# Optimization experiments

Measured on AMD Instinct MI355X. Metric: run time of the kernel, lower is better.

Reference implementation:

```python
import jax, jax.numpy as jnp
from jax import lax
import numpy as np

D_MODEL = 1024
D_STATE = 16
D_CONV = 4
EXPAND = 2
D_INNER = EXPAND * D_MODEL          # 2048
DT_RANK = D_MODEL // 16             # 64 (mamba 'auto' dt_rank)
B, L = 1, 1024


def setup_inputs() -> dict:
    key = jax.random.key(0)
    ks = jax.random.split(key, 8)

    def nrm(k, shape, s=0.02):
        return jax.random.normal(k, shape, jnp.float32) * s

    def mamba_params(kbase):
        k = jax.random.split(kbase, 7)
        return {
            'in_w': nrm(k[0], (2 * D_INNER, D_MODEL)),            # in_proj (no bias)
            'conv_w': nrm(k[1], (D_INNER, 1, D_CONV), 0.1),       # depthwise causal conv
            'conv_b': nrm(k[2], (D_INNER,), 0.1),
            'xproj_w': nrm(k[3], (DT_RANK + 2 * D_STATE, D_INNER)),
            'dt_w': nrm(k[4], (D_INNER, DT_RANK), 0.1),
            'dt_b': nrm(k[5], (D_INNER,), 0.1),
            'Alog': jnp.log(jnp.broadcast_to(jnp.arange(1., D_STATE + 1, dtype=jnp.float32), (D_INNER, D_STATE))),
            'Dp': jnp.ones((D_INNER,), jnp.float32),
            'out_w': nrm(k[6], (D_MODEL, D_INNER)),
        }

    fw = mamba_params(ks[0])
    bw = mamba_params(ks[1])
    inp = {'x': jax.random.normal(ks[2], (B, L, D_MODEL), jnp.float32)}
    for n, p in fw.items():
        inp['fw_' + n] = p
    for n, p in bw.items():
        inp['bw_' + n] = p
    inp['proj_w'] = nrm(ks[3], (D_MODEL, 2 * D_MODEL))
    inp['proj_b'] = jnp.zeros((D_MODEL,), jnp.float32)
    inp['ln_w'] = jnp.ones((D_MODEL,), jnp.float32)
    inp['ln_b'] = jnp.zeros((D_MODEL,), jnp.float32)
    return inp


def _mamba(x, in_w, conv_w, conv_b, xproj_w, dt_w, dt_b, Alog, Dp, out_w):
    # x: [B, L, d_model]
    xz = x @ in_w.T                                    # [B, L, 2*d_inner]
    xi, z = jnp.split(xz, 2, axis=-1)
    # causal depthwise conv over time
    xc = lax.conv_general_dilated(jnp.swapaxes(xi, 1, 2), conv_w, (1,),
                                  [(D_CONV - 1, 0)], feature_group_count=D_INNER)
    u = jnp.swapaxes(jax.nn.silu(xc + conv_b[None, :, None]), 1, 2)   # [B, L, d_inner]
    x_dbl = u @ xproj_w.T                              # [B, L, dt_rank + 2*d_state]
    dt = x_dbl[..., :DT_RANK]
    Bm = x_dbl[..., DT_RANK:DT_RANK + D_STATE]
    Cm = x_dbl[..., DT_RANK + D_STATE:]
    delta = jax.nn.softplus(dt @ dt_w.T + dt_b)        # [B, L, d_inner]
    A = -jnp.exp(Alog)                                 # [d_inner, d_state]
    dA = jnp.exp(jnp.einsum('bld,dn->bldn', delta, A))
    dBu = jnp.einsum('bld,bln,bld->bldn', delta, Bm, u)

    def step(h, inputs):
        a, b, c = inputs                               # a,b: [B,D,N]; c: [B,N]
        h = a * h + b
        return h, jnp.einsum('bdn,bn->bd', h, c)

    h0 = jnp.zeros((x.shape[0], D_INNER, D_STATE), x.dtype)
    _, ys = lax.scan(step, h0, (jnp.moveaxis(dA, 1, 0), jnp.moveaxis(dBu, 1, 0), jnp.moveaxis(Cm, 1, 0)))
    y = jnp.moveaxis(ys, 0, 1) + u * Dp                # [B, L, d_inner]
    return (y * jax.nn.silu(z)) @ out_w.T              # [B, L, d_model]


def _block(x,
           fw_in_w, fw_conv_w, fw_conv_b, fw_xproj_w, fw_dt_w, fw_dt_b, fw_Alog, fw_Dp, fw_out_w,
           bw_in_w, bw_conv_w, bw_conv_b, bw_xproj_w, bw_dt_w, bw_dt_b, bw_Alog, bw_Dp, bw_out_w,
           proj_w, proj_b, ln_w, ln_b):
    out_fw = _mamba(x, fw_in_w, fw_conv_w, fw_conv_b, fw_xproj_w, fw_dt_w, fw_dt_b, fw_Alog, fw_Dp, fw_out_w) + x
    xb = jnp.flip(x, axis=1)
    out_bw = jnp.flip(_mamba(xb, bw_in_w, bw_conv_w, bw_conv_b, bw_xproj_w, bw_dt_w, bw_dt_b, bw_Alog, bw_Dp, bw_out_w) + xb, axis=1)
    out = jnp.concatenate([out_fw, out_bw], axis=-1) @ proj_w.T + proj_b
    mu = out.mean(-1, keepdims=True)
    var = out.var(-1, keepdims=True)
    return (out - mu) / jnp.sqrt(var + 1e-5) * ln_w + ln_b


def reference(x,
              fw_in_w, fw_conv_w, fw_conv_b, fw_xproj_w, fw_dt_w, fw_dt_b, fw_Alog, fw_Dp, fw_out_w,
              bw_in_w, bw_conv_w, bw_conv_b, bw_xproj_w, bw_dt_w, bw_dt_b, bw_Alog, bw_Dp, bw_out_w,
              proj_w, proj_b, ln_w, ln_b):
    return _block(x,
                  fw_in_w, fw_conv_w, fw_conv_b, fw_xproj_w, fw_dt_w, fw_dt_b, fw_Alog, fw_Dp, fw_out_w,
                  bw_in_w, bw_conv_w, bw_conv_b, bw_xproj_w, bw_dt_w, bw_dt_b, bw_Alog, bw_Dp, bw_out_w,
                  proj_w, proj_b, ln_w, ln_b)
```

## Files before the change

### kernel.cpp

```cpp
#include <hip/hip_runtime.h>

typedef __bf16 bf16;
typedef __bf16 bf16x8 __attribute__((ext_vector_type(8)));
typedef float  f32x4  __attribute__((ext_vector_type(4)));

#define L_SEQ 1024
#define DM    1024
#define DI    2048
#define DTR   64
#define DSTATE 16
#define XD    96
#define NC    64
#define CS    16

__device__ __forceinline__ float bf2f(bf16 v){ return (float)v; }
__device__ __forceinline__ bf16  f2bf(float v){ return (bf16)v; }

__device__ __forceinline__ void gl_lds16(const bf16* g, bf16* l) {
  __builtin_amdgcn_global_load_lds(
      (const __attribute__((address_space(1))) unsigned int*)g,
      (__attribute__((address_space(3))) unsigned int*)l, 16, 0, 0);
}

#define OFF_X      0L
#define OFF_INW    1048576L
#define OFF_XPROJ  9437184L
#define OFF_DTW    9830400L
#define OFF_OUTW   10092544L
#define OFF_PROJW  14286848L
#define CVT_TOTAL  16384000L

__global__ __launch_bounds__(256) void cvt_k(
    const float* __restrict__ x,
    const float* __restrict__ inw0, const float* __restrict__ inw1,
    const float* __restrict__ xp0,  const float* __restrict__ xp1,
    const float* __restrict__ dt0,  const float* __restrict__ dt1,
    const float* __restrict__ ow0,  const float* __restrict__ ow1,
    const float* __restrict__ pw,   bf16* __restrict__ wb)
{
  long i = ((long)blockIdx.x * 256 + threadIdx.x) * 8;
  if (i >= CVT_TOTAL) return;
  const float* src; long off;
  if      (i < OFF_INW)                 { src = x;    off = i - OFF_X; }
  else if (i < OFF_INW + 4194304L)      { src = inw0; off = i - OFF_INW; }
  else if (i < OFF_XPROJ)               { src = inw1; off = i - (OFF_INW + 4194304L); }
  else if (i < OFF_XPROJ + 196608L)     { src = xp0;  off = i - OFF_XPROJ; }
  else if (i < OFF_DTW)                 { src = xp1;  off = i - (OFF_XPROJ + 196608L); }
  else if (i < OFF_DTW + 131072L)       { src = dt0;  off = i - OFF_DTW; }
  else if (i < OFF_OUTW)                { src = dt1;  off = i - (OFF_DTW + 131072L); }
  else if (i < OFF_OUTW + 2097152L)     { src = ow0;  off = i - OFF_OUTW; }
  else if (i < OFF_PROJW)               { src = ow1;  off = i - (OFF_OUTW + 2097152L); }
  else                                  { src = pw;   off = i - OFF_PROJW; }
  f32x4 v0 = *(const f32x4*)(src + off);
  f32x4 v1 = *(const f32x4*)(src + off + 4);
  bf16x8 t;
  #pragma unroll
  for (int q = 0; q < 4; q++) { t[q] = (bf16)v0[q]; t[4+q] = (bf16)v1[q]; }
  *(bf16x8*)(wb + i) = t;
}

template<int BM, int BN>
__global__ __launch_bounds__(256) void gemm_bt(
    const bf16* __restrict__ A, const bf16* __restrict__ B0, const bf16* __restrict__ B1,
    void* __restrict__ Cv, void* __restrict__ Cv2, int splitN,
    int M, int N, int K, int lda, int ldb, int ldc,
    long aOffZ, long cOffZ,
    const float* __restrict__ bias0, const float* __restrict__ bias1,
    int flipA1, int writeBf16, int act,
    const float* __restrict__ xF, int fuseRes)
{
  constexpr int WM = BM / 2, WN = BN / 2;
  constexpr int MI = WM / 16, NJ = WN / 16;
  constexpr int ACALLS = BM / 32;
  constexpr int BCALLS = BN / 32;

  const int tid  = threadIdx.x;
  const int z    = blockIdx.z;
  const bf16*  Bp   = z ? B1 : B0;
  const float* bias = z ? bias1 : bias0;
  const int flip = z ? flipA1 : 0;
  const int bm = blockIdx.x * BM;
  const int bn = blockIdx.y * BN;

  __shared__ bf16 As[BM * 64];
  __shared__ bf16 Bs[BN * 64];

  f32x4 acc[MI][NJ];
  #pragma unroll
  for (int i=0;i<MI;i++)
    #pragma unroll
    for (int j=0;j<NJ;j++) { acc[i][j][0]=0.f; acc[i][j][1]=0.f; acc[i][j][2]=0.f; acc[i][j][3]=0.f; }

  const int wave = tid >> 6;
  const int lane = tid & 63;
  const int wm = (wave >> 1) * WM;
  const int wn = (wave & 1) * WN;
  const int fr  = lane & 15;
  const int frx = fr & 7;
  const int kqc = lane >> 4;

  const bf16* aSrc[ACALLS];
  int aOff[ACALLS];
  #pragma unroll
  for (int t = 0; t < ACALLS; t++) {
    int s = (wave * ACALLS + t) * 64 + lane;
    int r = s >> 3;
    int j = (s & 7) ^ (r & 7);
    int ar = bm + r;
    int agr = flip ? (M - 1 - ar) : ar;
    aSrc[t] = A + (long)z * aOffZ + (long)agr * lda + j * 8;
    aOff[t] = (wave * ACALLS + t) * 512;
  }
  const bf16* bSrc[BCALLS];
  int bOff[BCALLS];
  #pragma unroll
  for (int t = 0; t < BCALLS; t++) {
    int s = (wave * BCALLS + t) * 64 + lane;
    int r = s >> 3;
    int j = (s & 7) ^ (r & 7);
    int br = bn + r; if (br > N - 1) br = N - 1;
    bSrc[t] = Bp + (long)br * ldb + j * 8;
    bOff[t] = (wave * BCALLS + t) * 512;
  }

  for (int k0 = 0; k0 < K; k0 += 64) {
    #pragma unroll
    for (int t = 0; t < ACALLS; t++) gl_lds16(aSrc[t] + k0, &As[aOff[t]]);
    #pragma unroll
    for (int t = 0; t < BCALLS; t++) gl_lds16(bSrc[t] + k0, &Bs[bOff[t]]);
    __syncthreads();

    #pragma unroll
    for (int ks8 = 0; ks8 < 8; ks8 += 4) {
      bf16x8 af[MI], bfr[NJ];
      #pragma unroll
      for (int i=0;i<MI;i++) {
        int row = wm + i*16 + fr;
        af[i]  = *(const bf16x8*)&As[(row * 8 + ((ks8 + kqc) ^ frx)) * 8];
      }
      #pragma unroll
      for (int j=0;j<NJ;j++) {
        int row = wn + j*16 + fr;
        bfr[j] = *(const bf16x8*)&Bs[(row * 8 + ((ks8 + kqc) ^ frx)) * 8];
      }
      #pragma unroll
      for (int i=0;i<MI;i++)
        #pragma unroll
        for (int j=0;j<NJ;j++)
          acc[i][j] = __builtin_amdgcn_mfma_f32_16x16x32_bf16(af[i], bfr[j], acc[i][j], 0, 0, 0);
    }
    __syncthreads();
  }

  const int rr = (lane >> 4) * 4;
  const int cc = lane & 15;
  #pragma unroll
  for (int i=0;i<MI;i++) {
    #pragma unroll
    for (int j=0;j<NJ;j++) {
      int gn = bn + wn + j*16 + cc;
      if (gn >= N) continue;
      float bv = bias ? bias[gn] : 0.f;
      #pragma unroll
      for (int r=0;r<4;r++) {
        int gm = bm + wm + i*16 + rr + r;
        float v = acc[i][j][r] + bv;
        if (fuseRes) {
          long row = z ? (long)(M - 1 - gm) : (long)gm;
          float o = v + xF[row * DM + gn];
          ((bf16*)Cv)[row * (2 * DM) + (long)z * DM + gn] = f2bf(o);
        } else {
          if (act == 1) v = fmaxf(v, 0.f) + __logf(1.f + __expf(-fabsf(v)));
          int gn2 = gn;
          void* Cp = Cv;
          if (gn >= splitN) { gn2 = gn - splitN; Cp = Cv2; }
          long idx = (long)z * cOffZ + (long)gm * ldc + gn2;
          if (writeBf16) ((bf16*)Cp)[idx] = f2bf(v);
          else           ((float*)Cp)[idx] = v;
        }
      }
    }
  }
}

__global__ __launch_bounds__(256) void conv_silu_k(
    const bf16* __restrict__ xi, const float* __restrict__ cw0, const float* __restrict__ cw1,
    const float* __restrict__ cb0, const float* __restrict__ cb1, bf16* __restrict__ u)
{
  int gid = blockIdx.x * 256 + threadIdx.x;
  int dir = gid >> 18;
  int rem = gid & ((1 << 18) - 1);
  int l = rem >> 8;
  int d0 = (rem & 255) * 8;
  const float* w = dir ? cw1 : cw0;
  const float* b = dir ? cb1 : cb0;
  const bf16* xid = xi + (long)dir * L_SEQ * DI;
  float acc[8];
  #pragma unroll
  for (int q = 0; q < 8; q++) acc[q] = b[d0 + q];
  #pragma unroll
  for (int j = 0; j < 4; j++) {
    int ll = l - 3 + j;
    if (ll < 0) continue;
    bf16x8 xv = *(const bf16x8*)(xid + (long)ll * DI + d0);
    #pragma unroll
    for (int q = 0; q < 8; q++) acc[q] += w[(d0 + q) * 4 + j] * bf2f(xv[q]);
  }
  bf16x8 o;
  #pragma unroll
  for (int q = 0; q < 8; q++) {
    float s = acc[q] / (1.f + __expf(-acc[q]));
    o[q] = f2bf(s);
  }
  *(bf16x8*)(u + (long)dir * L_SEQ * DI + (long)l * DI + d0) = o;
}

__global__ __launch_bounds__(256) void scan_p1(
    const bf16* __restrict__ delta, const bf16* __restrict__ u, const bf16* __restrict__ xdbl,
    const float* __restrict__ Alog0, const float* __restrict__ Alog1,
    bf16* __restrict__ hout, float* __restrict__ sumd)
{
  const int tid = threadIdx.x;
  const int c   = blockIdx.y;
  const int dir = blockIdx.z;
  const int d   = blockIdx.x * 256 + tid;
  const float* Alog = dir ? Alog1 : Alog0;
  const bf16* dl = delta + (long)dir * L_SEQ * DI;
  const bf16* ud = u     + (long)dir * L_SEQ * DI;
  const bf16* xd = xdbl  + (long)dir * L_SEQ * XD;
  const int l0 = c * CS;

  __shared__ float lb[CS][16];
  {
    int ll = tid >> 4, n = tid & 15;
    lb[ll][n] = bf2f(xd[(long)(l0 + ll) * XD + DTR + n]);
  }

  float dl_r[CS], uu_r[CS];
  #pragma unroll
  for (int s = 0; s < CS; s++) {
    dl_r[s] = bf2f(dl[(long)(l0 + s) * DI + d]);
    uu_r[s] = bf2f(ud[(long)(l0 + s) * DI + d]);
  }
  __syncthreads();

  float An[16], h[16];
  #pragma unroll
  for (int n = 0; n < 16; n++) { An[n] = -__expf(Alog[d * 16 + n]); h[n] = 0.f; }
  float sd = 0.f;

  #pragma unroll
  for (int ll = 0; ll < CS; ll++) {
    float dlt = dl_r[ll];
    sd += dlt;
    float du = dlt * uu_r[ll];
    #pragma unroll
    for (int n = 0; n < 16; n++) {
      float a = __expf(dlt * An[n]);
      h[n] = h[n] * a + du * lb[ll][n];
    }
  }

  bf16* hp = hout + (((long)dir * NC + c) * DI + d) * 16;
  bf16x8 o0, o1;
  #pragma unroll
  for (int n = 0; n < 8; n++) { o0[n] = f2bf(h[n]); o1[n] = f2bf(h[8 + n]); }
  *(bf16x8*)hp = o0;
  *(bf16x8*)(hp + 8) = o1;
  sumd[((long)dir * NC + c) * DI + d] = sd;
}

__global__ __launch_bounds__(256) void scan_p2(
    const float* __restrict__ Alog0, const float* __restrict__ Alog1,
    bf16* hout, const float* __restrict__ sumd)
{
  int g = blockIdx.x * 256 + threadIdx.x;
  int dir = g >> 15;
  int rem = g & 32767;
  int d = rem >> 4;
  int n = rem & 15;
  const float* Alog = dir ? Alog1 : Alog0;
  float An = -__expf(Alog[d * 16 + n]);
  float hs = 0.f;
  #pragma unroll 4
  for (int c = 0; c < NC; c++) {
    long base = ((long)dir * NC + c) * DI + d;
    float tmp = bf2f(hout[base * 16 + n]);
    float P = __expf(An * sumd[base]);
    hout[base * 16 + n] = f2bf(hs);
    hs = P * hs + tmp;
  }
}

__global__ __launch_bounds__(256) void scan_p3(
    const bf16* delta, const bf16* zb, const bf16* u, const bf16* __restrict__ xdbl,
    const float* __restrict__ Alog0, const float* __restrict__ Alog1,
    const float* __restrict__ Dp0, const float* __restrict__ Dp1,
    const bf16* __restrict__ hout, bf16* g)
{
  const int tid = threadIdx.x;
  const int c   = blockIdx.y;
  const int dir = blockIdx.z;
  const int d   = blockIdx.x * 256 + tid;
  const float* Alog = dir ? Alog1 : Alog0;
  const float* Dp   = dir ? Dp1 : Dp0;
  const bf16* dl = delta + (long)dir * L_SEQ * DI;
  const bf16* zd = zb    + (long)dir * L_SEQ * DI;
  const bf16* ud = u     + (long)dir * L_SEQ * DI;
  const bf16* xd = xdbl  + (long)dir * L_SEQ * XD;
  bf16* gd = g + (long)dir * L_SEQ * DI;
  const int l0 = c * CS;

  __shared__ float lb[CS][16];
  __shared__ float lc[CS][16];
  {
    int i = tid * 2;
    int ll = i >> 5, j = i & 31;
    const bf16* p = xd + (long)(l0 + ll) * XD + DTR + j;
    float v0 = bf2f(p[0]), v1 = bf2f(p[1]);
    if (j < 16) { lb[ll][j] = v0; lb[ll][j + 1] = v1; }
    else        { lc[ll][j - 16] = v0; lc[ll][j - 15] = v1; }
  }

  float dl_r[CS], uu_r[CS], zv_r[CS];
  #pragma unroll
  for (int s = 0; s < CS; s++) {
    dl_r[s] = bf2f(dl[(long)(l0 + s) * DI + d]);
    zv_r[s] = bf2f(zd[(long)(l0 + s) * DI + d]);
    uu_r[s] = bf2f(ud[(long)(l0 + s) * DI + d]);
  }
  const bf16* hp = hout + (((long)dir * NC + c) * DI + d) * 16;
  bf16x8 h0 = *(const bf16x8*)hp;
  bf16x8 h1 = *(const bf16x8*)(hp + 8);
  __syncthreads();

  float An[16], h[16];
  #pragma unroll
  for (int n = 0; n < 16; n++) {
    An[n] = -__expf(Alog[d * 16 + n]);
    h[n] = bf2f(n < 8 ? h0[n & 7] : h1[n & 7]);
  }
  const float Dpv = Dp[d];

  #pragma unroll
  for (int ll = 0; ll < CS; ll++) {
    float dlt = dl_r[ll];
    float du = dlt * uu_r[ll];
    float y = 0.f;
    #pragma unroll
    for (int n = 0; n < 16; n++) {
      float a = __expf(dlt * An[n]);
      h[n] = h[n] * a + du * lb[ll][n];
      y += h[n] * lc[ll][n];
    }
    y += uu_r[ll] * Dpv;
    float zv = zv_r[ll];
    float sz = zv / (1.f + __expf(-zv));
    gd[(long)(l0 + ll) * DI + d] = f2bf(y * sz);
  }
}

__global__ __launch_bounds__(256) void ln_k(
    const float* __restrict__ fin, const float* __restrict__ pb,
    const float* __restrict__ lnw, const float* __restrict__ lnb, float* __restrict__ out)
{
  int row = blockIdx.x;
  int tid = threadIdx.x;
  float v[4]; float s1 = 0.f, s2 = 0.f;
  #pragma unroll
  for (int j = 0; j < 4; j++) {
    int c = tid + j * 256;
    v[j] = fin[(long)row * DM + c] + pb[c];
    s1 += v[j]; s2 += v[j] * v[j];
  }
  #pragma unroll
  for (int off = 32; off; off >>= 1) { s1 += __shfl_down(s1, off); s2 += __shfl_down(s2, off); }
  __shared__ float red[8];
  int wave = tid >> 6, lane = tid & 63;
  if (lane == 0) { red[wave] = s1; red[4 + wave] = s2; }
  __syncthreads();
  float t1 = red[0] + red[1] + red[2] + red[3];
  float t2 = red[4] + red[5] + red[6] + red[7];
  float mu = t1 / DM;
  float var = t2 / DM - mu * mu;
  float inv = rsqrtf(var + 1e-5f);
  #pragma unroll
  for (int j = 0; j < 4; j++) {
    int c = tid + j * 256;
    out[(long)row * DM + c] = (v[j] - mu) * inv * lnw[c] + lnb[c];
  }
}

extern "C" void kernel_launch(void* const* d_in, const int* in_sizes, int n_in,
                              void* d_out, int out_size, void* d_ws, size_t ws_size,
                              hipStream_t stream)
{
  const float* x         = (const float*)d_in[0];
  const float* fw_conv_w = (const float*)d_in[2];
  const float* fw_conv_b = (const float*)d_in[3];
  const float* fw_dt_b   = (const float*)d_in[6];
  const float* fw_Alog   = (const float*)d_in[7];
  const float* fw_Dp     = (const float*)d_in[8];
  const float* bw_conv_w = (const float*)d_in[11];
  const float* bw_conv_b = (const float*)d_in[12];
  const float* bw_dt_b   = (const float*)d_in[15];
  const float* bw_Alog   = (const float*)d_in[16];
  const float* bw_Dp     = (const float*)d_in[17];
  const float* proj_b    = (const float*)d_in[20];
  const float* ln_w      = (const float*)d_in[21];
  const float* ln_b      = (const float*)d_in[22];

  char* ws = (char*)d_ws;
  const size_t MB = 1024 * 1024;
  bf16*  xi    = (bf16*)(ws + 0);
  bf16*  zb    = (bf16*)(ws + 8 * MB);
  bf16*  u     = (bf16*)(ws + 16 * MB);
  bf16*  xdbl  = (bf16*)(ws + 24 * MB);
  float* sumd  = (float*)(ws + 25 * MB);
  bf16*  hout  = (bf16*)(ws + 26 * MB);
  bf16*  wb    = (bf16*)(ws + 34 * MB);
  bf16*  g     = u;
  bf16*  delta = xi;
  bf16*  fused = (bf16*)(ws + 0);
  float* fin   = (float*)(ws + 4 * MB);

  bf16* xb     = wb + OFF_X;
  bf16* inw    = wb + OFF_INW;
  bf16* xprojw = wb + OFF_XPROJ;
  bf16* dtw    = wb + OFF_DTW;
  bf16* outw   = wb + OFF_OUTW;
  bf16* projw  = wb + OFF_PROJW;

  dim3 blk(256);
  const int BIGN = 1 << 30;

  cvt_k<<<(CVT_TOTAL / 8 + 255) / 256, blk, 0, stream>>>(
      x, (const float*)d_in[1], (const float*)d_in[10],
      (const float*)d_in[4], (const float*)d_in[13],
      (const float*)d_in[5], (const float*)d_in[14],
      (const float*)d_in[9], (const float*)d_in[18],
      (const float*)d_in[19], wb);

  gemm_bt<64,128><<<dim3(16, 32, 2), blk, 0, stream>>>(
      xb, inw, inw + 4194304L, (void*)xi, (void*)zb, 2048,
      1024, 4096, 1024, 1024, 1024, 2048,
      0L, (long)1024 * 2048, nullptr, nullptr, 1, 1, 0, nullptr, 0);

  conv_silu_k<<<2048, blk, 0, stream>>>(xi, fw_conv_w, bw_conv_w, fw_conv_b, bw_conv_b, u);

  gemm_bt<32,64><<<dim3(32, 2, 2), blk, 0, stream>>>(
      u, xprojw, xprojw + 196608L, (void*)xdbl, nullptr, BIGN,
      1024, 96, 2048, 2048, 2048, 96,
      (long)1024 * 2048, (long)1024 * 96, nullptr, nullptr, 0, 1, 0, nullptr, 0);

  gemm_bt<32,64><<<dim3(32, 32, 2), blk, 0, stream>>>(
      xdbl, dtw, dtw + 131072L, (void*)delta, nullptr, BIGN,
      1024, 2048, 64, 96, 64, 2048,
      (long)1024 * 96, (long)1024 * 2048, fw_dt_b, bw_dt_b, 0, 1, 1, nullptr, 0);

  scan_p1<<<dim3(8, NC, 2), blk, 0, stream>>>(delta, u, xdbl, fw_Alog, bw_Alog, hout, sumd);
  scan_p2<<<dim3(256), blk, 0, stream>>>(fw_Alog, bw_Alog, hout, sumd);
  scan_p3<<<dim3(8, NC, 2), blk, 0, stream>>>(delta, zb, u, xdbl, fw_Alog, bw_Alog,
                                              fw_Dp, bw_Dp, hout, g);

  gemm_bt<32,64><<<dim3(32, 16, 2), blk, 0, stream>>>(
      g, outw, outw + 2097152L, (void*)fused, nullptr, BIGN,
      1024, 1024, 2048, 2048, 2048, 1024,
      (long)1024 * 2048, 0L, nullptr, nullptr, 0, 1, 0, x, 1);

  gemm_bt<32,64><<<dim3(32, 16, 1), blk, 0, stream>>>(
      fused, projw, projw, (void*)fin, nullptr, BIGN,
      1024, 1024, 2048, 2048, 2048, 1024,
      0L, 0L, nullptr, nullptr, 0, 0, 0, nullptr, 0);

  ln_k<<<1024, blk, 0, stream>>>(fin, proj_b, ln_w, ln_b, (float*)d_out);
}
```

Measured before the change: 324.3 us.

## Fuse causal conv+SiLU into x_proj GEMM A-tile load; retile in_proj GEMM

Removes the standalone conv_silu kernel. Each block of the x_proj GEMM now computes the depthwise causal conv plus SiLU for its A tile directly from xi and writes it into shared memory. Only the blockIdx.y==0 blocks also write u to global memory for the later scan. This saves one launch and one round trip of u, but the conv is recomputed in both N-blocks and the x_proj GEMM has only 128 blocks, so its A loads are not pipelined. Separately, the in_proj GEMM tile changes from 64x128 to 64x64, doubling its grid.

```diff
diff --git a/kernel.cpp b/kernel.cpp
--- a/kernel.cpp
+++ b/kernel.cpp
@@ -183,36 +183,114 @@
   }
 }
 
-__global__ __launch_bounds__(256) void conv_silu_k(
-    const bf16* __restrict__ xi, const float* __restrict__ cw0, const float* __restrict__ cw1,
-    const float* __restrict__ cb0, const float* __restrict__ cb1, bf16* __restrict__ u)
-{
-  int gid = blockIdx.x * 256 + threadIdx.x;
-  int dir = gid >> 18;
-  int rem = gid & ((1 << 18) - 1);
-  int l = rem >> 8;
-  int d0 = (rem & 255) * 8;
-  const float* w = dir ? cw1 : cw0;
-  const float* b = dir ? cb1 : cb0;
-  const bf16* xid = xi + (long)dir * L_SEQ * DI;
-  float acc[8];
-  #pragma unroll
-  for (int q = 0; q < 8; q++) acc[q] = b[d0 + q];
-  #pragma unroll
-  for (int j = 0; j < 4; j++) {
-    int ll = l - 3 + j;
-    if (ll < 0) continue;
-    bf16x8 xv = *(const bf16x8*)(xid + (long)ll * DI + d0);
-    #pragma unroll
-    for (int q = 0; q < 8; q++) acc[q] += w[(d0 + q) * 4 + j] * bf2f(xv[q]);
-  }
-  bf16x8 o;
-  #pragma unroll
-  for (int q = 0; q < 8; q++) {
-    float s = acc[q] / (1.f + __expf(-acc[q]));
-    o[q] = f2bf(s);
-  }
-  *(bf16x8*)(u + (long)dir * L_SEQ * DI + (long)l * DI + d0) = o;
+__global__ __launch_bounds__(256) void gemm_xproj_conv(
+    const bf16* __restrict__ xi, const bf16* __restrict__ B0, const bf16* __restrict__ B1,
+    const float* __restrict__ cw0, const float* __restrict__ cw1,
+    const float* __restrict__ cb0, const float* __restrict__ cb1,
+    bf16* __restrict__ xdbl, bf16* __restrict__ u)
+{
+  constexpr int BM = 32, BN = 64, NB = 96;
+  const int tid = threadIdx.x;
+  const int z   = blockIdx.z;
+  const bf16* Bp  = z ? B1 : B0;
+  const float* cw = z ? cw1 : cw0;
+  const float* cb = z ? cb1 : cb0;
+  const bf16* xid = xi + (long)z * L_SEQ * DI;
+  bf16* ud        = u  + (long)z * L_SEQ * DI;
+  const int bm = blockIdx.x * BM;
+  const int bn = blockIdx.y * BN;
+
+  __shared__ bf16 As[BM * 64];
+  __shared__ bf16 Bs[BN * 64];
+
+  f32x4 acc[1][2];
+  acc[0][0][0]=0.f; acc[0][0][1]=0.f; acc[0][0][2]=0.f; acc[0][0][3]=0.f;
+  acc[0][1] = acc[0][0];
+
+  const int wave = tid >> 6;
+  const int lane = tid & 63;
+  const int wm = (wave >> 1) * 16;
+  const int wn = (wave & 1) * 32;
+  const int fr  = lane & 15;
+  const int frx = fr & 7;
+  const int kqc = lane >> 4;
+
+  const int ar  = tid >> 3;
+  const int ac0 = (tid & 7) * 8;
+  const int al  = bm + ar;
+  const int aswz = ((ac0 >> 3) ^ (ar & 7)) * 8 + ar * 64;
+  const bool writeU = (blockIdx.y == 0);
+
+  const bf16* bSrc[2];
+  int bOff[2];
+  #pragma unroll
+  for (int t = 0; t < 2; t++) {
+    int s = (wave * 2 + t) * 64 + lane;
+    int r = s >> 3;
+    int j = (s & 7) ^ (r & 7);
+    int br = bn + r; if (br > NB - 1) br = NB - 1;
+    bSrc[t] = Bp + (long)br * DI + j * 8;
+    bOff[t] = (wave * 2 + t) * 512;
+  }
+
+  for (int k0 = 0; k0 < DI; k0 += 64) {
+    #pragma unroll
+    for (int t = 0; t < 2; t++) gl_lds16(bSrc[t] + k0, &Bs[bOff[t]]);
+    {
+      int d0 = k0 + ac0;
+      float a[8];
+      #pragma unroll
+      for (int q = 0; q < 8; q++) a[q] = cb[d0 + q];
+      f32x4 wq[8];
+      #pragma unroll
+      for (int q = 0; q < 8; q++) wq[q] = *(const f32x4*)(cw + (d0 + q) * 4);
+      #pragma unroll
+      for (int j = 0; j < 4; j++) {
+        int ll = al - 3 + j;
+        if (ll >= 0) {
+          bf16x8 xv = *(const bf16x8*)(xid + (long)ll * DI + d0);
+          #pragma unroll
+          for (int q = 0; q < 8; q++) a[q] += wq[q][j] * bf2f(xv[q]);
+        }
+      }
+      bf16x8 o;
+      #pragma unroll
+      for (int q = 0; q < 8; q++) {
+        float s = a[q] / (1.f + __expf(-a[q]));
+        o[q] = f2bf(s);
+      }
+      *(bf16x8*)&As[aswz] = o;
+      if (writeU) *(bf16x8*)(ud + (long)al * DI + d0) = o;
+    }
+    __syncthreads();
+
+    #pragma unroll
+    for (int ks8 = 0; ks8 < 8; ks8 += 4) {
+      bf16x8 af, bfr[2];
+      af = *(const bf16x8*)&As[((wm + fr) * 8 + ((ks8 + kqc) ^ frx)) * 8];
+      #pragma unroll
+      for (int j = 0; j < 2; j++) {
+        int row = wn + j * 16 + fr;
+        bfr[j] = *(const bf16x8*)&Bs[(row * 8 + ((ks8 + kqc) ^ frx)) * 8];
+      }
+      acc[0][0] = __builtin_amdgcn_mfma_f32_16x16x32_bf16(af, bfr[0], acc[0][0], 0, 0, 0);
+      acc[0][1] = __builtin_amdgcn_mfma_f32_16x16x32_bf16(af, bfr[1], acc[0][1], 0, 0, 0);
+    }
+    __syncthreads();
+  }
+
+  const int rr = (lane >> 4) * 4;
+  const int cc = lane & 15;
+  #pragma unroll
+  for (int j = 0; j < 2; j++) {
+    int gn = bn + wn + j * 16 + cc;
+    if (gn >= NB) continue;
+    #pragma unroll
+    for (int r = 0; r < 4; r++) {
+      int gm = bm + wm + rr + r;
+      xdbl[(long)z * L_SEQ * XD + (long)gm * XD + gn] = f2bf(acc[0][j][r]);
+    }
+  }
 }
 
 __global__ __launch_bounds__(256) void scan_p1(
@@ -441,17 +519,14 @@
       (const float*)d_in[9], (const float*)d_in[18],
       (const float*)d_in[19], wb);
 
-  gemm_bt<64,128><<<dim3(16, 32, 2), blk, 0, stream>>>(
+  gemm_bt<64,64><<<dim3(16, 64, 2), blk, 0, stream>>>(
       xb, inw, inw + 4194304L, (void*)xi, (void*)zb, 2048,
       1024, 4096, 1024, 1024, 1024, 2048,
       0L, (long)1024 * 2048, nullptr, nullptr, 1, 1, 0, nullptr, 0);
 
-  conv_silu_k<<<2048, blk, 0, stream>>>(xi, fw_conv_w, bw_conv_w, fw_conv_b, bw_conv_b, u);
-
-  gemm_bt<32,64><<<dim3(32, 2, 2), blk, 0, stream>>>(
-      u, xprojw, xprojw + 196608L, (void*)xdbl, nullptr, BIGN,
-      1024, 96, 2048, 2048, 2048, 96,
-      (long)1024 * 2048, (long)1024 * 96, nullptr, nullptr, 0, 1, 0, nullptr, 0);
+  gemm_xproj_conv<<<dim3(32, 2, 2), blk, 0, stream>>>(
+      xi, xprojw, xprojw + 196608L,
+      fw_conv_w, bw_conv_w, fw_conv_b, bw_conv_b, xdbl, u);
 
   gemm_bt<32,64><<<dim3(32, 32, 2), blk, 0, stream>>>(
       xdbl, dtw, dtw + 131072L, (void*)delta, nullptr, BIGN,
```

After: 357.0 us. 1.1x slower.
